# Optimization experiments

Measured on AMD Instinct MI355X. Metric: run time of the kernel, lower is better.

## Reference

```python
import jax, jax.numpy as jnp
import numpy as np

B, C, CK, HW = 4, 512, 512, 64
EPS = 1e-5


def conv1x1(x, w, b):
    # 1x1 conv == per-pixel linear: x [b,c,h,w], w [o,c], b [o]
    return jnp.einsum('bchw,oc->bohw', x, w) + b[None, :, None, None]


def mean_variance_norm(feat):
    # torch .var(dim=2) defaults to unbiased (ddof=1)
    b, c = feat.shape[:2]
    flat = feat.reshape(b, c, -1)
    mean = flat.mean(axis=-1)
    std = jnp.sqrt(flat.var(axis=-1, ddof=1) + EPS)
    return (feat - mean[:, :, None, None]) / std[:, :, None, None]


def setup_inputs() -> dict:
    key = jax.random.key(0)
    ks = jax.random.split(key, 10)
    sc_k = 1.0 / np.sqrt(CK)
    sc_c = 1.0 / np.sqrt(C)
    return {
        'content': jax.random.normal(ks[0], (B, C, HW, HW), jnp.float32),
        'style': jax.random.normal(ks[1], (B, C, HW, HW), jnp.float32),
        'content_key': jax.random.normal(ks[2], (B, CK, HW, HW), jnp.float32),
        'style_key': jax.random.normal(ks[3], (B, CK, HW, HW), jnp.float32),
        'f_w': jax.random.normal(ks[4], (CK, CK), jnp.float32) * sc_k,
        'f_b': jnp.zeros((CK,), jnp.float32),
        'g_w': jax.random.normal(ks[5], (CK, CK), jnp.float32) * sc_k,
        'g_b': jnp.zeros((CK,), jnp.float32),
        'h_w': jax.random.normal(ks[6], (C, C), jnp.float32) * sc_c,
        'h_b': jnp.zeros((C,), jnp.float32),
        'w_mix': jnp.ones((2,), jnp.float32),
    }


def reference(content, style, content_key, style_key,
              f_w, f_b, g_w, g_b, h_w, h_b, w_mix):
    Fm = conv1x1(content_key, f_w, f_b)   # [b,ck,h,w]
    Gm = conv1x1(style_key, g_w, g_b)     # [b,ck,hs,ws]
    Hm = conv1x1(style, h_w, h_b)         # [b,c,hs,ws]
    b, ck, h, w = Fm.shape
    c = Hm.shape[1]

    G = Gm.reshape(b, ck, -1)                                # [b,ck,Ns]
    style_flat = Hm.reshape(b, c, -1).transpose(0, 2, 1)      # [b,Ns,c]
    Fq = Fm.reshape(b, ck, -1).transpose(0, 2, 1)             # [b,Nc,ck]

    raw_attn = jnp.einsum('bnk,bkm->bnm', Fq, G)              # [b,Nc,Ns]
    attn_dense = jax.nn.softmax(raw_attn, axis=-1)
    attn_sparse = jax.nn.softmax(jax.nn.relu(raw_attn), axis=-1)

    wts = jax.nn.softmax(w_mix)  # exp(w)/sum(exp(w))
    S = jax.nn.softmax(attn_dense * wts[0] + attn_sparse * wts[1], axis=-1)

    mean = jnp.einsum('bnm,bmc->bnc', S, style_flat)          # E[x]
    second = jnp.einsum('bnm,bmc->bnc', S, style_flat ** 2)   # E[x^2]
    std = jnp.sqrt(jax.nn.relu(second - mean ** 2))

    mean = mean.reshape(b, h, w, c).transpose(0, 3, 1, 2)
    std = std.reshape(b, h, w, c).transpose(0, 3, 1, 2)
    return std * mean_variance_norm(content) + mean
```

## Files before the change

kernel.cpp:

```cpp
#include <hip/hip_runtime.h>
#include <hip/hip_bf16.h>
#include <hip/hip_fp16.h>
#include <stdint.h>

typedef float f32x4 __attribute__((ext_vector_type(4)));
typedef short short8 __attribute__((ext_vector_type(8)));
typedef unsigned short u16;

static __device__ __forceinline__ u16 f2bf(float f) {
    __hip_bfloat16 h = __float2bfloat16(f);
    return *reinterpret_cast<const u16*>(&h);
}
static __device__ __forceinline__ u16 f2h(float f) {
    __half h = __float2half(f);
    return *reinterpret_cast<const u16*>(&h);
}
static __device__ __forceinline__ float h2f(u16 b) {
    __half h = *reinterpret_cast<const __half*>(&b);
    return __half2float(h);
}

static __device__ __forceinline__ void gload16(const void* g, void* l) {
    __builtin_amdgcn_global_load_lds((const __attribute__((address_space(1))) void*)g,
                                     (__attribute__((address_space(3))) void*)l, 16, 0, 0);
}

__global__ void k_cast3(const float* __restrict__ a, const float* __restrict__ b,
                        const float* __restrict__ c, u16* __restrict__ oa,
                        u16* __restrict__ ob, u16* __restrict__ oc) {
    int i = blockIdx.x * blockDim.x + threadIdx.x;
    int which = i >> 16, j = i & 65535;
    const float* in = (which == 0) ? a : (which == 1) ? b : c;
    u16* out = (which == 0) ? oa : (which == 1) ? ob : oc;
    float4 v = ((const float4*)in)[j];
    ushort4 o;
    o.x = f2bf(v.x); o.y = f2bf(v.y); o.z = f2bf(v.z); o.w = f2bf(v.w);
    ((ushort4*)out)[j] = o;
}

__global__ __launch_bounds__(256) void k_transpose(const float* __restrict__ in, u16* __restrict__ out) {
    __shared__ float t[64][65];
    int b = blockIdx.z;
    int c0 = blockIdx.y * 64;
    int n0 = blockIdx.x * 64;
    const float* ip = in + ((size_t)b * 512 + c0) * 4096 + n0;
#pragma unroll
    for (int i = 0; i < 16; ++i) {
        int idx = threadIdx.x + i * 256;
        int cl = idx >> 6, nl = idx & 63;
        t[cl][nl] = ip[(size_t)cl * 4096 + nl];
    }
    __syncthreads();
    u16* op = out + ((size_t)b * 4096 + n0) * 512 + c0;
#pragma unroll
    for (int i = 0; i < 16; ++i) {
        int idx = threadIdx.x + i * 256;
        int nr = idx >> 6, cc = idx & 63;
        op[(size_t)nr * 512 + cc] = f2bf(t[cc][nr]);
    }
}

__global__ __launch_bounds__(256) void k_cstats(const float* __restrict__ content, float* __restrict__ cstat) {
    int c = blockIdx.x, b = blockIdx.y;
    const float4* r4 = (const float4*)(content + ((size_t)b * 512 + c) * 4096);
    float s = 0.f, ss = 0.f;
    for (int i = threadIdx.x; i < 1024; i += 256) {
        float4 v = r4[i];
        s += v.x + v.y + v.z + v.w;
        ss += v.x * v.x + v.y * v.y + v.z * v.z + v.w * v.w;
    }
#pragma unroll
    for (int k = 1; k < 64; k <<= 1) { s += __shfl_xor(s, k); ss += __shfl_xor(ss, k); }
    __shared__ float ls[4], lss[4];
    int w = threadIdx.x >> 6;
    if ((threadIdx.x & 63) == 0) { ls[w] = s; lss[w] = ss; }
    __syncthreads();
    if (threadIdx.x == 0) {
        s = ls[0] + ls[1] + ls[2] + ls[3];
        ss = lss[0] + lss[1] + lss[2] + lss[3];
        float mu = s / 4096.f;
        float var = (ss - 4096.f * mu * mu) / 4095.f;
        cstat[((size_t)b * 512 + c) * 2] = mu;
        cstat[((size_t)b * 512 + c) * 2 + 1] = rsqrtf(var + 1e-5f);
    }
}

__global__ __launch_bounds__(256) void k_convP(const u16* __restrict__ XT, const u16* __restrict__ Wb,
                                               const float* __restrict__ bias, u16* __restrict__ out) {
    int bid = blockIdx.x;
    int b = (bid & 7) >> 1;
    int u = ((bid & 1) << 8) | (bid >> 3);
    int n0 = (u & 63) * 64, o0 = (u >> 6) * 64;
    int lane = threadIdx.x & 63, w = threadIdx.x >> 6;
    int l15 = lane & 15, l4 = lane >> 4;
    const u16* ap = XT + ((size_t)b * 4096 + n0 + w * 16 + l15) * 512 + l4 * 8;
    f32x4 acc[4] = {{0,0,0,0},{0,0,0,0},{0,0,0,0},{0,0,0,0}};
#pragma unroll
    for (int kk = 0; kk < 16; ++kk) {
        short8 a = *(const short8*)(ap + kk * 32);
#pragma unroll
        for (int bo = 0; bo < 4; ++bo) {
            const u16* bp = Wb + ((size_t)(o0 + bo * 16 + l15)) * 512 + kk * 32 + l4 * 8;
            short8 bb = *(const short8*)bp;
            acc[bo] = __builtin_amdgcn_mfma_f32_16x16x32_bf16(a, bb, acc[bo], 0, 0, 0);
        }
    }
#pragma unroll
    for (int bo = 0; bo < 4; ++bo) {
        float bv = bias[o0 + bo * 16 + l15];
#pragma unroll
        for (int r = 0; r < 4; ++r) {
            int n = n0 + w * 16 + l4 * 4 + r;
            out[((size_t)b * 4096 + n) * 512 + o0 + bo * 16 + l15] = f2bf(acc[bo][r] + bv);
        }
    }
}

__global__ __launch_bounds__(256) void k_convH(const u16* __restrict__ ST, const u16* __restrict__ Wb,
                                               const float* __restrict__ bias, u16* __restrict__ out) {
    int bid = blockIdx.x;
    int b = (bid & 7) >> 1;
    int u = ((bid & 1) << 8) | (bid >> 3);
    int m0 = (u & 63) * 64, o0 = (u >> 6) * 64;
    int lane = threadIdx.x & 63, w = threadIdx.x >> 6;
    int l15 = lane & 15, l4 = lane >> 4;
    const u16* ap = Wb + ((size_t)(o0 + w * 16 + l15)) * 512 + l4 * 8;
    f32x4 acc[4] = {{0,0,0,0},{0,0,0,0},{0,0,0,0},{0,0,0,0}};
#pragma unroll
    for (int kk = 0; kk < 16; ++kk) {
        short8 a = *(const short8*)(ap + kk * 32);
#pragma unroll
        for (int mb = 0; mb < 4; ++mb) {
            const u16* bp = ST + ((size_t)b * 4096 + m0 + mb * 16 + l15) * 512 + kk * 32 + l4 * 8;
            short8 bb = *(const short8*)bp;
            acc[mb] = __builtin_amdgcn_mfma_f32_16x16x32_bf16(a, bb, acc[mb], 0, 0, 0);
        }
    }
#pragma unroll
    for (int r = 0; r < 4; ++r) {
        int o = o0 + w * 16 + l4 * 4 + r;
        float bv = bias[o];
#pragma unroll
        for (int mb = 0; mb < 4; ++mb) {
            float v = acc[mb][r] + bv;
            size_t base = ((size_t)b * 1024 + o) * 4096 + m0 + mb * 16 + l15;
            out[base] = f2bf(v);
            out[base + (size_t)512 * 4096] = f2bf(v * v);
        }
    }
}

__global__ __launch_bounds__(512, 4) void k_attnA(
    const u16* __restrict__ Q, const u16* __restrict__ G,
    u16* __restrict__ Lg, float* __restrict__ stats) {

    __shared__ __align__(16) u16 gtile[2][32 * 512];
    __shared__ float smd[4][2][16], ssd_[4][2][16], smsp[4][2][16], sssp[4][2][16];

    int bid = blockIdx.x;
    int b = (bid & 7) >> 1;
    int g = bid >> 3;
    int qt = ((bid & 1) << 5) | (g >> 1);
    int half = g & 1;
    int n0 = qt * 64;
    int kv0 = half * 2048;
    int lane = threadIdx.x & 63, w = threadIdx.x >> 6;
    int l15 = lane & 15, l4 = lane >> 4;
    int R = w >> 1, MB = w & 1;

    const u16* qp = Q + ((size_t)b * 4096 + n0 + R * 16 + l15) * 512 + l4 * 8;
    short8 q[16];
#pragma unroll
    for (int kk = 0; kk < 16; ++kk) q[kk] = *(const short8*)(qp + kk * 32);

    const char* gbat = (const char*)(G + (size_t)b * 4096 * 512);

#define STAGEA(buf, mc)                                                                \
    {                                                                                  \
        _Pragma("unroll")                                                              \
        for (int j = 0; j < 4; ++j) {                                                  \
            int row = j * 8 + w;                                                       \
            const char* src = gbat + ((size_t)(kv0 + (mc) * 32 + row)) * 1024          \
                              + ((lane * 16) ^ ((row & 7) << 4));                      \
            gload16(src, (char*)&gtile[buf][0] + row * 1024);                          \
        }                                                                              \
    }

    float md[4], sd[4], ms[4], ss[4];
#pragma unroll
    for (int r = 0; r < 4; ++r) { md[r] = -1e30f; sd[r] = 0.f; ms[r] = -1e30f; ss[r] = 0.f; }

    STAGEA(0, 0);
    __syncthreads();
    for (int mc = 0; mc < 64; ++mc) {
        int buf = mc & 1;
        if (mc < 63) STAGEA(buf ^ 1, mc + 1);
        f32x4 acc = {0, 0, 0, 0};
        const char* gt = (const char*)&gtile[buf][0];
#pragma unroll
        for (int kk = 0; kk < 16; ++kk) {
            int row = MB * 16 + l15;
            int y = (kk * 64 + l4 * 16) ^ ((row & 7) << 4);
            short8 gg = *(const short8*)(gt + row * 1024 + y);
            acc = __builtin_amdgcn_mfma_f32_16x16x32_bf16(q[kk], gg, acc, 0, 0, 0);
        }
#pragma unroll
        for (int r = 0; r < 4; ++r) {
            float v = acc[r];
            float mn = fmaxf(md[r], v);
            sd[r] = sd[r] * __expf(md[r] - mn) + __expf(v - mn);
            md[r] = mn;
            float vs = fmaxf(v, 0.f);
            mn = fmaxf(ms[r], vs);
            ss[r] = ss[r] * __expf(ms[r] - mn) + __expf(vs - mn);
            ms[r] = mn;
            int qg = n0 + R * 16 + l4 * 4 + r;
            Lg[((size_t)b * 4096 + qg) * 4096 + kv0 + mc * 32 + MB * 16 + l15] = f2h(v);
        }
        __syncthreads();
    }

#pragma unroll
    for (int r = 0; r < 4; ++r) {
#pragma unroll
        for (int k = 1; k < 16; k <<= 1) {
            float mo = __shfl_xor(md[r], k), so = __shfl_xor(sd[r], k);
            float mn = fmaxf(md[r], mo);
            sd[r] = sd[r] * __expf(md[r] - mn) + so * __expf(mo - mn);
            md[r] = mn;
            mo = __shfl_xor(ms[r], k); so = __shfl_xor(ss[r], k);
            mn = fmaxf(ms[r], mo);
            ss[r] = ss[r] * __expf(ms[r] - mn) + so * __expf(mo - mn);
            ms[r] = mn;
        }
    }
    if (l15 == 0) {
#pragma unroll
        for (int r = 0; r < 4; ++r) {
            int row = l4 * 4 + r;
            smd[R][MB][row] = md[r]; ssd_[R][MB][row] = sd[r];
            smsp[R][MB][row] = ms[r]; sssp[R][MB][row] = ss[r];
        }
    }
    __syncthreads();
    if (MB == 0 && l15 == 0) {
#pragma unroll
        for (int r = 0; r < 4; ++r) {
            int row = l4 * 4 + r;
            float m0_ = smd[R][0][row], s0_ = ssd_[R][0][row];
            float m1_ = smd[R][1][row], s1_ = ssd_[R][1][row];
            float mn = fmaxf(m0_, m1_);
            float Sd = s0_ * __expf(m0_ - mn) + s1_ * __expf(m1_ - mn);
            float Md = mn;
            m0_ = smsp[R][0][row]; s0_ = sssp[R][0][row];
            m1_ = smsp[R][1][row]; s1_ = sssp[R][1][row];
            mn = fmaxf(m0_, m1_);
            float Ss = s0_ * __expf(m0_ - mn) + s1_ * __expf(m1_ - mn);
            float Ms = mn;
            int qg = n0 + R * 16 + l4 * 4 + r;
            float4 st = {Md, Sd, Ms, Ss};
            *(float4*)(stats + (((size_t)b * 4096 + qg) * 2 + half) * 4) = st;
        }
    }
#undef STAGEA
}

__global__ __launch_bounds__(512, 4) void k_attnB(
    const u16* __restrict__ Lg, const u16* __restrict__ H,
    const float* __restrict__ stats, const float* __restrict__ wmix,
    const float* __restrict__ content, const float* __restrict__ cstat,
    float* __restrict__ out) {

    __shared__ __align__(16) u16 et[2][4096];
    __shared__ float zrow[64];

    int bid = blockIdx.x;
    int b = (bid & 7) >> 1;
    int g = bid >> 3;
    int qt = ((bid & 1) << 5) | (g >> 1);
    int cs = g & 1;
    int n0 = qt * 64;
    int lane = threadIdx.x & 63, w = threadIdx.x >> 6;
    int l15 = lane & 15, l4 = lane >> 4;

    float wa = wmix[0], wbv = wmix[1];
    float wmx = fmaxf(wa, wbv);
    float e0 = __expf(wa - wmx), e1 = __expf(wbv - wmx);
    float w0 = e0 / (e0 + e1), w1 = e1 / (e0 + e1);

    int qlocal = w * 8 + (lane >> 3);
    int kvl = (lane & 7) * 8;
    float md, isd, ms, iss;
    {
        const float* sp = stats + (((size_t)b * 4096 + n0 + qlocal) * 2) * 4;
        float4 s0 = *(const float4*)sp;
        float4 s1 = *(const float4*)(sp + 4);
        float mn = fmaxf(s0.x, s1.x);
        float S = s0.y * __expf(s0.x - mn) + s1.y * __expf(s1.x - mn);
        md = mn; isd = 1.f / S;
        mn = fmaxf(s0.z, s1.z);
        S = s0.w * __expf(s0.z - mn) + s1.w * __expf(s1.z - mn);
        ms = mn; iss = 1.f / S;
    }
    const u16* lgrow = Lg + ((size_t)b * 4096 + n0 + qlocal) * 4096 + kvl;
    unsigned ewbyte = (unsigned)(qlocal * 128) + (((unsigned)(lane & 7) * 16) ^ ((unsigned)(qlocal & 7) << 4));

    float z = 0.f;

#define PRODUCE(buf, mc)                                                               \
    {                                                                                  \
        short8 L8 = *(const short8*)(lgrow + (size_t)(mc) * 64);                       \
        short8 ebf;                                                                    \
        _Pragma("unroll")                                                              \
        for (int j = 0; j < 8; ++j) {                                                  \
            float v = h2f((u16)L8[j]);                                                 \
            float ed = __expf(v - md) * isd;                                           \
            float es = __expf(fmaxf(v, 0.f) - ms) * iss;                               \
            float e = __expf(w0 * ed + w1 * es);                                       \
            z += e;                                                                    \
            ebf[j] = (short)f2bf(e);                                                   \
        }                                                                              \
        *(short8*)((char*)&et[buf][0] + ewbyte) = ebf;                                 \
    }

    f32x4 pv[16];
#pragma unroll
    for (int i = 0; i < 16; ++i) pv[i] = (f32x4){0, 0, 0, 0};

    PRODUCE(0, 0);
    __syncthreads();
    for (int mc = 0; mc < 64; ++mc) {
        int buf = mc & 1;
        if (mc < 63) PRODUCE(buf ^ 1, mc + 1);
        const char* eb = (const char*)&et[buf][0];
        const u16* hb = H + (size_t)b * 1024 * 4096 + (size_t)mc * 64 + l4 * 8;
#pragma unroll
        for (int ks = 0; ks < 2; ++ks) {
            short8 af[4];
#pragma unroll
            for (int qf = 0; qf < 4; ++qf) {
                int qq = qf * 16 + l15;
                int y = (ks * 64 + l4 * 16) ^ ((qq & 7) << 4);
                af[qf] = *(const short8*)(eb + qq * 128 + y);
            }
#pragma unroll
            for (int cf = 0; cf < 4; ++cf) {
                int c = (cf < 2) ? (cs * 256 + w * 32 + cf * 16 + l15)
                                 : (512 + cs * 256 + w * 32 + (cf - 2) * 16 + l15);
                short8 hh = *(const short8*)(hb + (size_t)c * 4096 + ks * 32);
#pragma unroll
                for (int qf = 0; qf < 4; ++qf)
                    pv[qf * 4 + cf] = __builtin_amdgcn_mfma_f32_16x16x32_bf16(af[qf], hh, pv[qf * 4 + cf], 0, 0, 0);
            }
        }
        __syncthreads();
    }

    z += __shfl_xor(z, 1);
    z += __shfl_xor(z, 2);
    z += __shfl_xor(z, 4);
    if ((lane & 7) == 0) zrow[qlocal] = z;
    __syncthreads();

#pragma unroll
    for (int qf = 0; qf < 4; ++qf) {
        float iz[4];
#pragma unroll
        for (int r = 0; r < 4; ++r)
            iz[r] = 1.f / zrow[qf * 16 + l4 * 4 + r];
#pragma unroll
        for (int cf = 0; cf < 2; ++cf) {
            int c = cs * 256 + w * 32 + cf * 16 + l15;
            float mu = cstat[((size_t)b * 512 + c) * 2];
            float rstd = cstat[((size_t)b * 512 + c) * 2 + 1];
            const float* cp = content + ((size_t)b * 512 + c) * 4096 + n0 + qf * 16 + l4 * 4;
            float* op = out + ((size_t)b * 512 + c) * 4096 + n0 + qf * 16 + l4 * 4;
            float4 cv = *(const float4*)cp;
            float4 ov;
#pragma unroll
            for (int r = 0; r < 4; ++r) {
                float mean = pv[qf * 4 + cf][r] * iz[r];
                float sec = pv[qf * 4 + cf + 2][r] * iz[r];
                float stdv = sqrtf(fmaxf(sec - mean * mean, 0.f));
                (&ov.x)[r] = stdv * ((&cv.x)[r] - mu) * rstd + mean;
            }
            *(float4*)op = ov;
        }
    }
#undef PRODUCE
}

extern "C" void kernel_launch(void* const* d_in, const int* in_sizes, int n_in,
                              void* d_out, int out_size, void* d_ws, size_t ws_size,
                              hipStream_t stream) {
    (void)in_sizes; (void)n_in; (void)out_size; (void)ws_size;
    const float* content = (const float*)d_in[0];
    const float* style   = (const float*)d_in[1];
    const float* ckey    = (const float*)d_in[2];
    const float* skey    = (const float*)d_in[3];
    const float* f_w = (const float*)d_in[4];
    const float* f_b = (const float*)d_in[5];
    const float* g_w = (const float*)d_in[6];
    const float* g_b = (const float*)d_in[7];
    const float* h_w = (const float*)d_in[8];
    const float* h_b = (const float*)d_in[9];
    const float* wmix = (const float*)d_in[10];
    float* out = (float*)d_out;

    const size_t MiB = 1048576;
    char* ws = (char*)d_ws;
    u16* ckT = (u16*)(ws + 0);
    u16* skT = (u16*)(ws + 16 * MiB);
    u16* stT = (u16*)(ws + 32 * MiB);
    u16* fwB = (u16*)(ws + 48 * MiB);
    u16* gwB = (u16*)(ws + 48 * MiB + 524288);
    u16* hwB = (u16*)(ws + 49 * MiB);
    float* cst = (float*)(ws + 49 * MiB + 524288);
    u16* Qb  = (u16*)(ws + 50 * MiB);
    u16* Gb  = (u16*)(ws + 66 * MiB);
    u16* Hb  = (u16*)(ws + 0);
    u16* Lg  = (u16*)(ws + 82 * MiB);
    float* stats = (float*)(ws + 210 * MiB);

    k_cast3<<<768, 256, 0, stream>>>(f_w, g_w, h_w, fwB, gwB, hwB);
    k_transpose<<<dim3(64, 8, 4), 256, 0, stream>>>(ckey, ckT);
    k_transpose<<<dim3(64, 8, 4), 256, 0, stream>>>(skey, skT);
    k_transpose<<<dim3(64, 8, 4), 256, 0, stream>>>(style, stT);
    k_cstats<<<dim3(512, 4), 256, 0, stream>>>(content, cst);
    k_convP<<<dim3(2048), 256, 0, stream>>>(ckT, fwB, f_b, Qb);
    k_convP<<<dim3(2048), 256, 0, stream>>>(skT, gwB, g_b, Gb);
    k_convH<<<dim3(2048), 256, 0, stream>>>(stT, hwB, h_b, Hb);
    k_attnA<<<dim3(512), 512, 0, stream>>>(Qb, Gb, Lg, stats);
    k_attnB<<<dim3(512), 512, 0, stream>>>(Lg, Hb, stats, wmix, content, cst, out);
}
```

Before: 784.9 us.

## Transpose attention MFMA so each lane owns one query row and vectorize logit stores

Swaps the MFMA operands in the score kernel so each lane's four accumulator values belong to one query row across four key positions. This lets the online dense/sparse softmax statistics run on scalars per lane instead of four rows, and lets the fp16 logits be written as one packed 4-element store instead of four scattered scalar stores. The cross-lane reduction shrinks to shuffles across lane groups. The block-index mapping to batch, query tile and key half also changes in both attention kernels, which alters which blocks run concurrently and their cache behaviour.

Result: faster. 760.4 us (-3.1%).

```diff
diff --git a/kernel.cpp b/kernel.cpp
--- a/kernel.cpp
+++ b/kernel.cpp
@@ -5,6 +5,7 @@
 
 typedef float f32x4 __attribute__((ext_vector_type(4)));
 typedef short short8 __attribute__((ext_vector_type(8)));
+typedef unsigned short ushort4_t __attribute__((ext_vector_type(4)));
 typedef unsigned short u16;
 
 static __device__ __forceinline__ u16 f2bf(float f) {
@@ -159,9 +160,8 @@
 
     int bid = blockIdx.x;
     int b = (bid & 7) >> 1;
-    int g = bid >> 3;
-    int qt = ((bid & 1) << 5) | (g >> 1);
-    int half = g & 1;
+    int half = bid & 1;
+    int qt = bid >> 3;
     int n0 = qt * 64;
     int kv0 = half * 2048;
     int lane = threadIdx.x & 63, w = threadIdx.x >> 6;
@@ -174,6 +174,7 @@
     for (int kk = 0; kk < 16; ++kk) q[kk] = *(const short8*)(qp + kk * 32);
 
     const char* gbat = (const char*)(G + (size_t)b * 4096 * 512);
+    size_t lgoff = ((size_t)b * 4096 + n0 + R * 16 + l15) * 4096 + kv0 + MB * 16 + l4 * 4;
 
 #define STAGEA(buf, mc)                                                                \
     {                                                                                  \
@@ -186,9 +187,7 @@
         }                                                                              \
     }
 
-    float md[4], sd[4], ms[4], ss[4];
-#pragma unroll
-    for (int r = 0; r < 4; ++r) { md[r] = -1e30f; sd[r] = 0.f; ms[r] = -1e30f; ss[r] = 0.f; }
+    float md = -1e30f, sd = 0.f, ms = -1e30f, ss = 0.f;
 
     STAGEA(0, 0);
     __syncthreads();
@@ -197,70 +196,59 @@
         if (mc < 63) STAGEA(buf ^ 1, mc + 1);
         f32x4 acc = {0, 0, 0, 0};
         const char* gt = (const char*)&gtile[buf][0];
+        int row = MB * 16 + l15;
 #pragma unroll
         for (int kk = 0; kk < 16; ++kk) {
-            int row = MB * 16 + l15;
             int y = (kk * 64 + l4 * 16) ^ ((row & 7) << 4);
             short8 gg = *(const short8*)(gt + row * 1024 + y);
-            acc = __builtin_amdgcn_mfma_f32_16x16x32_bf16(q[kk], gg, acc, 0, 0, 0);
-        }
-#pragma unroll
-        for (int r = 0; r < 4; ++r) {
-            float v = acc[r];
-            float mn = fmaxf(md[r], v);
-            sd[r] = sd[r] * __expf(md[r] - mn) + __expf(v - mn);
-            md[r] = mn;
-            float vs = fmaxf(v, 0.f);
-            mn = fmaxf(ms[r], vs);
-            ss[r] = ss[r] * __expf(ms[r] - mn) + __expf(vs - mn);
-            ms[r] = mn;
-            int qg = n0 + R * 16 + l4 * 4 + r;
-            Lg[((size_t)b * 4096 + qg) * 4096 + kv0 + mc * 32 + MB * 16 + l15] = f2h(v);
-        }
+            acc = __builtin_amdgcn_mfma_f32_16x16x32_bf16(gg, q[kk], acc, 0, 0, 0);
+        }
+        float v0 = acc[0], v1 = acc[1], v2 = acc[2], v3 = acc[3];
+        float mx = fmaxf(fmaxf(v0, v1), fmaxf(v2, v3));
+        float mn = fmaxf(md, mx);
+        sd = sd * __expf(md - mn) +
+             ((__expf(v0 - mn) + __expf(v1 - mn)) + (__expf(v2 - mn) + __expf(v3 - mn)));
+        md = mn;
+        float mns = fmaxf(ms, fmaxf(mx, 0.f));
+        ss = ss * __expf(ms - mns) +
+             ((__expf(fmaxf(v0, 0.f) - mns) + __expf(fmaxf(v1, 0.f) - mns)) +
+              (__expf(fmaxf(v2, 0.f) - mns) + __expf(fmaxf(v3, 0.f) - mns)));
+        ms = mns;
+        ushort4_t pk = {f2h(v0), f2h(v1), f2h(v2), f2h(v3)};
+        *(ushort4_t*)(Lg + lgoff + (size_t)mc * 32) = pk;
         __syncthreads();
     }
 
 #pragma unroll
-    for (int r = 0; r < 4; ++r) {
-#pragma unroll
-        for (int k = 1; k < 16; k <<= 1) {
-            float mo = __shfl_xor(md[r], k), so = __shfl_xor(sd[r], k);
-            float mn = fmaxf(md[r], mo);
-            sd[r] = sd[r] * __expf(md[r] - mn) + so * __expf(mo - mn);
-            md[r] = mn;
-            mo = __shfl_xor(ms[r], k); so = __shfl_xor(ss[r], k);
-            mn = fmaxf(ms[r], mo);
-            ss[r] = ss[r] * __expf(ms[r] - mn) + so * __expf(mo - mn);
-            ms[r] = mn;
-        }
-    }
-    if (l15 == 0) {
-#pragma unroll
-        for (int r = 0; r < 4; ++r) {
-            int row = l4 * 4 + r;
-            smd[R][MB][row] = md[r]; ssd_[R][MB][row] = sd[r];
-            smsp[R][MB][row] = ms[r]; sssp[R][MB][row] = ss[r];
-        }
-    }
-    __syncthreads();
-    if (MB == 0 && l15 == 0) {
-#pragma unroll
-        for (int r = 0; r < 4; ++r) {
-            int row = l4 * 4 + r;
-            float m0_ = smd[R][0][row], s0_ = ssd_[R][0][row];
-            float m1_ = smd[R][1][row], s1_ = ssd_[R][1][row];
-            float mn = fmaxf(m0_, m1_);
-            float Sd = s0_ * __expf(m0_ - mn) + s1_ * __expf(m1_ - mn);
-            float Md = mn;
-            m0_ = smsp[R][0][row]; s0_ = sssp[R][0][row];
-            m1_ = smsp[R][1][row]; s1_ = sssp[R][1][row];
-            mn = fmaxf(m0_, m1_);
-            float Ss = s0_ * __expf(m0_ - mn) + s1_ * __expf(m1_ - mn);
-            float Ms = mn;
-            int qg = n0 + R * 16 + l4 * 4 + r;
-            float4 st = {Md, Sd, Ms, Ss};
-            *(float4*)(stats + (((size_t)b * 4096 + qg) * 2 + half) * 4) = st;
-        }
+    for (int k = 16; k < 64; k <<= 1) {
+        float mo = __shfl_xor(md, k), so = __shfl_xor(sd, k);
+        float mn = fmaxf(md, mo);
+        sd = sd * __expf(md - mn) + so * __expf(mo - mn);
+        md = mn;
+        mo = __shfl_xor(ms, k); so = __shfl_xor(ss, k);
+        mn = fmaxf(ms, mo);
+        ss = ss * __expf(ms - mn) + so * __expf(mo - mn);
+        ms = mn;
+    }
+    if (l4 == 0) {
+        smd[R][MB][l15] = md; ssd_[R][MB][l15] = sd;
+        smsp[R][MB][l15] = ms; sssp[R][MB][l15] = ss;
+    }
+    __syncthreads();
+    if (MB == 0 && lane < 16) {
+        float m0_ = smd[R][0][l15], s0_ = ssd_[R][0][l15];
+        float m1_ = smd[R][1][l15], s1_ = ssd_[R][1][l15];
+        float mn = fmaxf(m0_, m1_);
+        float Sd = s0_ * __expf(m0_ - mn) + s1_ * __expf(m1_ - mn);
+        float Md = mn;
+        m0_ = smsp[R][0][l15]; s0_ = sssp[R][0][l15];
+        m1_ = smsp[R][1][l15]; s1_ = sssp[R][1][l15];
+        mn = fmaxf(m0_, m1_);
+        float Ss = s0_ * __expf(m0_ - mn) + s1_ * __expf(m1_ - mn);
+        float Ms = mn;
+        int qg = n0 + R * 16 + l15;
+        float4 st = {Md, Sd, Ms, Ss};
+        *(float4*)(stats + (((size_t)b * 4096 + qg) * 2 + half) * 4) = st;
     }
 #undef STAGEA
 }
@@ -276,9 +264,8 @@
 
     int bid = blockIdx.x;
     int b = (bid & 7) >> 1;
-    int g = bid >> 3;
-    int qt = ((bid & 1) << 5) | (g >> 1);
-    int cs = g & 1;
+    int cs = bid & 1;
+    int qt = bid >> 3;
     int n0 = qt * 64;
     int lane = threadIdx.x & 63, w = threadIdx.x >> 6;
     int l15 = lane & 15, l4 = lane >> 4;
```
